# Optimization experiments

Measured on AMD Instinct MI355X. Metric: run time of the kernel, lower is better.

The kernel has to match this reference:

```python
import jax, jax.numpy as jnp
import numpy as np

Q = 4096   # query_size = argument_size*relation_size*position_size = 32*16*8
L = 8192   # number of context rows


def setup_inputs() -> dict:
    key = jax.random.key(0)
    k1, k2, k3 = jax.random.split(key, 3)
    query = jax.random.normal(k1, (Q,), dtype=jnp.float32)
    context_vector = jax.random.normal(k2, (L, Q), dtype=jnp.float32)
    # torch Linear(2Q, Q, bias=False): weight shape [Q, 2Q], scaled init
    K_w = jax.random.normal(k3, (Q, 2 * Q), dtype=jnp.float32) / np.sqrt(2 * Q)
    return {"query": query, "context_vector": context_vector, "K_w": K_w}


def reference(query, context_vector, K_w):
    # score[l] = <context_vector[l], query>  -> [L]
    score = context_vector @ query
    attention = jax.nn.softmax(score, axis=0)          # softmax over L
    s_t = attention @ context_vector                    # [Q]
    gamma = jnp.concatenate([query, s_t])               # [2Q]
    return K_w @ gamma                                   # Linear(2Q -> Q), no bias
```

## Files before the change

### kernel.cpp

```cpp
#include <hip/hip_runtime.h>

#define Q 4096
#define L 8192

__global__ __launch_bounds__(256) void score_kernel(
    const float* __restrict__ ctx, const float* __restrict__ qvec,
    float* __restrict__ score)
{
    const int lane = threadIdx.x & 63;
    const int w    = blockIdx.x * 4 + (threadIdx.x >> 6);
    const float4* __restrict__ row = (const float4*)(ctx + (size_t)w * Q);
    const float4* __restrict__ qv  = (const float4*)qvec;

    float a0 = 0.f, a1 = 0.f, a2 = 0.f, a3 = 0.f;
    #pragma unroll
    for (int c = 0; c < 16; c += 4) {
        float4 x0 = row[(c + 0) * 64 + lane], y0 = qv[(c + 0) * 64 + lane];
        float4 x1 = row[(c + 1) * 64 + lane], y1 = qv[(c + 1) * 64 + lane];
        float4 x2 = row[(c + 2) * 64 + lane], y2 = qv[(c + 2) * 64 + lane];
        float4 x3 = row[(c + 3) * 64 + lane], y3 = qv[(c + 3) * 64 + lane];
        a0 = fmaf(x0.x, y0.x, a0); a0 = fmaf(x0.y, y0.y, a0);
        a0 = fmaf(x0.z, y0.z, a0); a0 = fmaf(x0.w, y0.w, a0);
        a1 = fmaf(x1.x, y1.x, a1); a1 = fmaf(x1.y, y1.y, a1);
        a1 = fmaf(x1.z, y1.z, a1); a1 = fmaf(x1.w, y1.w, a1);
        a2 = fmaf(x2.x, y2.x, a2); a2 = fmaf(x2.y, y2.y, a2);
        a2 = fmaf(x2.z, y2.z, a2); a2 = fmaf(x2.w, y2.w, a2);
        a3 = fmaf(x3.x, y3.x, a3); a3 = fmaf(x3.y, y3.y, a3);
        a3 = fmaf(x3.z, y3.z, a3); a3 = fmaf(x3.w, y3.w, a3);
    }
    float d = (a0 + a1) + (a2 + a3);
    #pragma unroll
    for (int off = 32; off > 0; off >>= 1) d += __shfl_down(d, off, 64);
    if (lane == 0) score[w] = d;
}

__global__ __launch_bounds__(1024) void softmax_kernel(
    const float* __restrict__ score, float* __restrict__ att)
{
    __shared__ float redm[16];
    __shared__ float reds[16];
    const int tid  = threadIdx.x;
    const int lane = tid & 63;
    const int wid  = tid >> 6;

    float m = -3.4e38f;
    for (int i = tid; i < L; i += 1024) m = fmaxf(m, score[i]);
    #pragma unroll
    for (int off = 32; off > 0; off >>= 1) m = fmaxf(m, __shfl_down(m, off, 64));
    if (lane == 0) redm[wid] = m;
    __syncthreads();
    float M = redm[0];
    #pragma unroll
    for (int w = 1; w < 16; ++w) M = fmaxf(M, redm[w]);

    float s = 0.f;
    for (int i = tid; i < L; i += 1024) s += __expf(score[i] - M);
    #pragma unroll
    for (int off = 32; off > 0; off >>= 1) s += __shfl_down(s, off, 64);
    if (lane == 0) reds[wid] = s;
    __syncthreads();
    float Z = 0.f;
    #pragma unroll
    for (int w = 0; w < 16; ++w) Z += reds[w];
    const float inv = 1.0f / Z;

    for (int i = tid; i < L; i += 1024) att[i] = __expf(score[i] - M) * inv;
}

__global__ __launch_bounds__(256) void wsum_kernel(
    const float* __restrict__ ctx, const float* __restrict__ att,
    float* __restrict__ partial)
{
    __shared__ float att_s[64];
    const int cc  = blockIdx.x & 3;
    const int rc  = blockIdx.x >> 2;
    const int tid = threadIdx.x;
    const int col = cc * 256 + tid;

    if (tid < 64) att_s[tid] = att[rc * 64 + tid];
    __syncthreads();

    const float4* __restrict__ cb = (const float4*)ctx;
    const int r0 = rc * 64;
    float4 acc = make_float4(0.f, 0.f, 0.f, 0.f);
    #pragma unroll 8
    for (int r = 0; r < 64; ++r) {
        const float a = att_s[r];
        float4 v = cb[(size_t)(r0 + r) * (Q / 4) + col];
        acc.x = fmaf(a, v.x, acc.x);
        acc.y = fmaf(a, v.y, acc.y);
        acc.z = fmaf(a, v.z, acc.z);
        acc.w = fmaf(a, v.w, acc.w);
    }
    ((float4*)partial)[(size_t)rc * (Q / 4) + col] = acc;
}

__global__ __launch_bounds__(256) void reduce_kernel(
    const float* __restrict__ partial, float* __restrict__ s_t)
{
    const int c4 = blockIdx.x * 256 + threadIdx.x;
    const float4* __restrict__ p = (const float4*)partial;
    float4 acc = make_float4(0.f, 0.f, 0.f, 0.f);
    #pragma unroll 8
    for (int b = 0; b < 128; ++b) {
        float4 v = p[(size_t)b * (Q / 4) + c4];
        acc.x += v.x; acc.y += v.y; acc.z += v.z; acc.w += v.w;
    }
    ((float4*)s_t)[c4] = acc;
}

__global__ __launch_bounds__(256) void out_kernel(
    const float* __restrict__ Kw, const float* __restrict__ qvec,
    const float* __restrict__ s_t, float* __restrict__ out)
{
    const int lane = threadIdx.x & 63;
    const int i    = blockIdx.x * 4 + (threadIdx.x >> 6);
    const float4* __restrict__ row = (const float4*)(Kw + (size_t)i * (2 * Q));
    const float4* __restrict__ qv  = (const float4*)qvec;
    const float4* __restrict__ sv  = (const float4*)s_t;

    float a0 = 0.f, a1 = 0.f, a2 = 0.f, a3 = 0.f;
    #pragma unroll
    for (int c = 0; c < 16; c += 4) {
        float4 x0 = row[(c + 0) * 64 + lane], y0 = qv[(c + 0) * 64 + lane];
        float4 x1 = row[(c + 1) * 64 + lane], y1 = qv[(c + 1) * 64 + lane];
        float4 x2 = row[(c + 2) * 64 + lane], y2 = qv[(c + 2) * 64 + lane];
        float4 x3 = row[(c + 3) * 64 + lane], y3 = qv[(c + 3) * 64 + lane];
        a0 = fmaf(x0.x, y0.x, a0); a0 = fmaf(x0.y, y0.y, a0);
        a0 = fmaf(x0.z, y0.z, a0); a0 = fmaf(x0.w, y0.w, a0);
        a1 = fmaf(x1.x, y1.x, a1); a1 = fmaf(x1.y, y1.y, a1);
        a1 = fmaf(x1.z, y1.z, a1); a1 = fmaf(x1.w, y1.w, a1);
        a2 = fmaf(x2.x, y2.x, a2); a2 = fmaf(x2.y, y2.y, a2);
        a2 = fmaf(x2.z, y2.z, a2); a2 = fmaf(x2.w, y2.w, a2);
        a3 = fmaf(x3.x, y3.x, a3); a3 = fmaf(x3.y, y3.y, a3);
        a3 = fmaf(x3.z, y3.z, a3); a3 = fmaf(x3.w, y3.w, a3);
    }
    #pragma unroll
    for (int c = 0; c < 16; c += 4) {
        float4 x0 = row[(16 + c + 0) * 64 + lane], y0 = sv[(c + 0) * 64 + lane];
        float4 x1 = row[(16 + c + 1) * 64 + lane], y1 = sv[(c + 1) * 64 + lane];
        float4 x2 = row[(16 + c + 2) * 64 + lane], y2 = sv[(c + 2) * 64 + lane];
        float4 x3 = row[(16 + c + 3) * 64 + lane], y3 = sv[(c + 3) * 64 + lane];
        a0 = fmaf(x0.x, y0.x, a0); a0 = fmaf(x0.y, y0.y, a0);
        a0 = fmaf(x0.z, y0.z, a0); a0 = fmaf(x0.w, y0.w, a0);
        a1 = fmaf(x1.x, y1.x, a1); a1 = fmaf(x1.y, y1.y, a1);
        a1 = fmaf(x1.z, y1.z, a1); a1 = fmaf(x1.w, y1.w, a1);
        a2 = fmaf(x2.x, y2.x, a2); a2 = fmaf(x2.y, y2.y, a2);
        a2 = fmaf(x2.z, y2.z, a2); a2 = fmaf(x2.w, y2.w, a2);
        a3 = fmaf(x3.x, y3.x, a3); a3 = fmaf(x3.y, y3.y, a3);
        a3 = fmaf(x3.z, y3.z, a3); a3 = fmaf(x3.w, y3.w, a3);
    }
    float d = (a0 + a1) + (a2 + a3);
    #pragma unroll
    for (int off = 32; off > 0; off >>= 1) d += __shfl_down(d, off, 64);
    if (lane == 0) out[i] = d;
}

extern "C" void kernel_launch(void* const* d_in, const int* in_sizes, int n_in,
                              void* d_out, int out_size, void* d_ws, size_t ws_size,
                              hipStream_t stream)
{
    const float* query = (const float*)d_in[0];
    const float* ctx   = (const float*)d_in[1];
    const float* Kw    = (const float*)d_in[2];
    float* out = (float*)d_out;

    float* ws      = (float*)d_ws;
    float* score   = ws;
    float* att     = ws + L;
    float* s_t     = ws + 2 * L;
    float* partial = ws + 2 * L + Q;

    score_kernel<<<2048, 256, 0, stream>>>(ctx, query, score);
    softmax_kernel<<<1, 1024, 0, stream>>>(score, att);
    wsum_kernel<<<512, 256, 0, stream>>>(ctx, att, partial);
    reduce_kernel<<<4, 256, 0, stream>>>(partial, s_t);
    out_kernel<<<1024, 256, 0, stream>>>(Kw, query, s_t, out);
}
```

Measured before the change: 83.16 us.

## Fuse softmax into chunked weighted-sum with online max and merge kernel

Removes the single-block softmax kernel by having each weighted-sum block compute a local max and exp-weights over 16 rows, storing per-block max and sum. A new merge kernel rescales and reduces the partials and normalizes. Rows are processed in four chunks, interleaving score and wsum so the second context read can hit cache. This adds more launches and a larger partial buffer to reduce.

```diff
diff --git a/kernel.cpp b/kernel.cpp
--- a/kernel.cpp
+++ b/kernel.cpp
@@ -2,13 +2,18 @@
 
 #define Q 4096
 #define L 8192
+#define NCHUNK 4
+#define CROWS (L / NCHUNK)
+#define WROWS 16
+#define NPB (L / WROWS)
+#define WCB 4
 
 __global__ __launch_bounds__(256) void score_kernel(
     const float* __restrict__ ctx, const float* __restrict__ qvec,
-    float* __restrict__ score)
+    float* __restrict__ score, int r0base)
 {
     const int lane = threadIdx.x & 63;
-    const int w    = blockIdx.x * 4 + (threadIdx.x >> 6);
+    const int w    = r0base + blockIdx.x * 4 + (threadIdx.x >> 6);
     const float4* __restrict__ row = (const float4*)(ctx + (size_t)w * Q);
     const float4* __restrict__ qv  = (const float4*)qvec;
 
@@ -34,79 +39,102 @@
     if (lane == 0) score[w] = d;
 }
 
-__global__ __launch_bounds__(1024) void softmax_kernel(
-    const float* __restrict__ score, float* __restrict__ att)
-{
-    __shared__ float redm[16];
-    __shared__ float reds[16];
-    const int tid  = threadIdx.x;
-    const int lane = tid & 63;
-    const int wid  = tid >> 6;
-
-    float m = -3.4e38f;
-    for (int i = tid; i < L; i += 1024) m = fmaxf(m, score[i]);
-    #pragma unroll
-    for (int off = 32; off > 0; off >>= 1) m = fmaxf(m, __shfl_down(m, off, 64));
-    if (lane == 0) redm[wid] = m;
-    __syncthreads();
-    float M = redm[0];
-    #pragma unroll
-    for (int w = 1; w < 16; ++w) M = fmaxf(M, redm[w]);
-
-    float s = 0.f;
-    for (int i = tid; i < L; i += 1024) s += __expf(score[i] - M);
-    #pragma unroll
-    for (int off = 32; off > 0; off >>= 1) s += __shfl_down(s, off, 64);
-    if (lane == 0) reds[wid] = s;
-    __syncthreads();
-    float Z = 0.f;
-    #pragma unroll
-    for (int w = 0; w < 16; ++w) Z += reds[w];
-    const float inv = 1.0f / Z;
-
-    for (int i = tid; i < L; i += 1024) att[i] = __expf(score[i] - M) * inv;
-}
-
 __global__ __launch_bounds__(256) void wsum_kernel(
-    const float* __restrict__ ctx, const float* __restrict__ att,
-    float* __restrict__ partial)
-{
-    __shared__ float att_s[64];
-    const int cc  = blockIdx.x & 3;
-    const int rc  = blockIdx.x >> 2;
+    const float* __restrict__ ctx, const float* __restrict__ score,
+    float* __restrict__ partial, float* __restrict__ m_arr,
+    float* __restrict__ Z_arr, int r0base)
+{
+    __shared__ float sc_s[WROWS];
+    __shared__ float w_s[WROWS];
+    const int cc  = blockIdx.x & (WCB - 1);
+    const int rg  = blockIdx.x / WCB;
+    const int r0  = r0base + rg * WROWS;
+    const int pb  = r0 / WROWS;
     const int tid = threadIdx.x;
+
+    if (tid < WROWS) sc_s[tid] = score[r0 + tid];
+    __syncthreads();
+    float m = sc_s[0];
+    #pragma unroll
+    for (int r = 1; r < WROWS; ++r) m = fmaxf(m, sc_s[r]);
+    if (tid < WROWS) w_s[tid] = __expf(sc_s[tid] - m);
+    __syncthreads();
+
     const int col = cc * 256 + tid;
-
-    if (tid < 64) att_s[tid] = att[rc * 64 + tid];
-    __syncthreads();
-
     const float4* __restrict__ cb = (const float4*)ctx;
-    const int r0 = rc * 64;
     float4 acc = make_float4(0.f, 0.f, 0.f, 0.f);
-    #pragma unroll 8
-    for (int r = 0; r < 64; ++r) {
-        const float a = att_s[r];
+    #pragma unroll
+    for (int r = 0; r < WROWS; ++r) {
+        const float a = w_s[r];
         float4 v = cb[(size_t)(r0 + r) * (Q / 4) + col];
         acc.x = fmaf(a, v.x, acc.x);
         acc.y = fmaf(a, v.y, acc.y);
         acc.z = fmaf(a, v.z, acc.z);
         acc.w = fmaf(a, v.w, acc.w);
     }
-    ((float4*)partial)[(size_t)rc * (Q / 4) + col] = acc;
-}
-
-__global__ __launch_bounds__(256) void reduce_kernel(
-    const float* __restrict__ partial, float* __restrict__ s_t)
-{
-    const int c4 = blockIdx.x * 256 + threadIdx.x;
+    ((float4*)partial)[(size_t)pb * (Q / 4) + col] = acc;
+
+    if (cc == 0 && tid == 0) {
+        float Z = 0.f;
+        #pragma unroll
+        for (int r = 0; r < WROWS; ++r) Z += w_s[r];
+        m_arr[pb] = m;
+        Z_arr[pb] = Z;
+    }
+}
+
+__global__ __launch_bounds__(256) void merge_kernel(
+    const float* __restrict__ partial, const float* __restrict__ m_arr,
+    const float* __restrict__ Z_arr, float* __restrict__ s_t)
+{
+    __shared__ float wc[NPB];
+    __shared__ float red[4];
+    __shared__ float4 sacc[16][16];
+    const int tid  = threadIdx.x;
+    const int lane = tid & 63;
+    const int wid  = tid >> 6;
+
+    float mv = fmaxf(m_arr[tid], m_arr[tid + 256]);
+    #pragma unroll
+    for (int off = 32; off > 0; off >>= 1) mv = fmaxf(mv, __shfl_down(mv, off, 64));
+    if (lane == 0) red[wid] = mv;
+    __syncthreads();
+    const float M = fmaxf(fmaxf(red[0], red[1]), fmaxf(red[2], red[3]));
+    __syncthreads();
+
+    const float w0 = __expf(m_arr[tid] - M);
+    const float w1 = __expf(m_arr[tid + 256] - M);
+    wc[tid] = w0; wc[tid + 256] = w1;
+    float zv = fmaf(w0, Z_arr[tid], w1 * Z_arr[tid + 256]);
+    #pragma unroll
+    for (int off = 32; off > 0; off >>= 1) zv += __shfl_down(zv, off, 64);
+    if (lane == 0) red[wid] = zv;
+    __syncthreads();
+    const float invZ = 1.f / (red[0] + red[1] + red[2] + red[3]);
+
+    const int cidx = tid & 15;
+    const int g    = tid >> 4;
+    const int c4   = blockIdx.x * 16 + cidx;
     const float4* __restrict__ p = (const float4*)partial;
     float4 acc = make_float4(0.f, 0.f, 0.f, 0.f);
-    #pragma unroll 8
-    for (int b = 0; b < 128; ++b) {
+    for (int b = g; b < NPB; b += 16) {
+        const float w = wc[b];
         float4 v = p[(size_t)b * (Q / 4) + c4];
-        acc.x += v.x; acc.y += v.y; acc.z += v.z; acc.w += v.w;
-    }
-    ((float4*)s_t)[c4] = acc;
+        acc.x = fmaf(w, v.x, acc.x); acc.y = fmaf(w, v.y, acc.y);
+        acc.z = fmaf(w, v.z, acc.z); acc.w = fmaf(w, v.w, acc.w);
+    }
+    sacc[g][cidx] = acc;
+    __syncthreads();
+    if (g == 0) {
+        float4 t = sacc[0][cidx];
+        #pragma unroll
+        for (int gg = 1; gg < 16; ++gg) {
+            float4 u = sacc[gg][cidx];
+            t.x += u.x; t.y += u.y; t.z += u.z; t.w += u.w;
+        }
+        t.x *= invZ; t.y *= invZ; t.z *= invZ; t.w *= invZ;
+        ((float4*)s_t)[c4] = t;
+    }
 }
 
 __global__ __launch_bounds__(256) void out_kernel(
@@ -167,13 +195,17 @@
 
     float* ws      = (float*)d_ws;
     float* score   = ws;
-    float* att     = ws + L;
-    float* s_t     = ws + 2 * L;
-    float* partial = ws + 2 * L + Q;
-
-    score_kernel<<<2048, 256, 0, stream>>>(ctx, query, score);
-    softmax_kernel<<<1, 1024, 0, stream>>>(score, att);
-    wsum_kernel<<<512, 256, 0, stream>>>(ctx, att, partial);
-    reduce_kernel<<<4, 256, 0, stream>>>(partial, s_t);
-    out_kernel<<<1024, 256, 0, stream>>>(Kw, query, s_t, out);
-}
+    float* m_arr   = ws + L;
+    float* Z_arr   = ws + L + NPB;
+    float* s_t     = ws + L + 2 * NPB;
+    float* partial = ws + L + 2 * NPB + Q;
+
+    for (int c = 0; c < NCHUNK; ++c) {
+        const int r0 = c * CROWS;
+        score_kernel<<<CROWS / 4, 256, 0, stream>>>(ctx, query, score, r0);
+        wsum_kernel<<<(CROWS / WROWS) * WCB, 256, 0, stream>>>(
+            ctx, score, partial, m_arr, Z_arr, r0);
+    }
+    merge_kernel<<<Q / 4 / 16, 256, 0, stream>>>(partial, m_arr, Z_arr, s_t);
+    out_kernel<<<Q / 4, 256, 0, stream>>>(Kw, query, s_t, out);
+}
```

After: 86.34 us. +3.8%, slower.

## Stage query vectors in LDS, halve wsum row chunk, parallelize partial reduction

Applied to the files above, without the earlier changes.

The score and output GEMV kernels now stage the shared query (and s_t) vectors in LDS once per block instead of each wave re-reading them from global memory. The weighted-sum kernel processes 32 rows per block instead of 64, doubling the block count for more parallelism but producing twice as many partial rows. The reduce kernel now uses 16 blocks, with four wave groups per block splitting the 256 partials and combining them through LDS, instead of 4 blocks of serial 128-row loops. This adds LDS traffic and barriers, and doubles the partial buffer writes and reads.

```diff
diff --git a/kernel.cpp b/kernel.cpp
--- a/kernel.cpp
+++ b/kernel.cpp
@@ -7,18 +7,26 @@
     const float* __restrict__ ctx, const float* __restrict__ qvec,
     float* __restrict__ score)
 {
-    const int lane = threadIdx.x & 63;
-    const int w    = blockIdx.x * 4 + (threadIdx.x >> 6);
+    __shared__ float4 qs[Q / 4];
+    const int tid  = threadIdx.x;
+    const int lane = tid & 63;
+    const int wid  = tid >> 6;
+    const float4* __restrict__ qv = (const float4*)qvec;
+
+    #pragma unroll
+    for (int k = 0; k < 4; ++k) qs[tid + k * 256] = qv[tid + k * 256];
+    __syncthreads();
+
+    const int w = blockIdx.x * 4 + wid;
     const float4* __restrict__ row = (const float4*)(ctx + (size_t)w * Q);
-    const float4* __restrict__ qv  = (const float4*)qvec;
 
     float a0 = 0.f, a1 = 0.f, a2 = 0.f, a3 = 0.f;
     #pragma unroll
     for (int c = 0; c < 16; c += 4) {
-        float4 x0 = row[(c + 0) * 64 + lane], y0 = qv[(c + 0) * 64 + lane];
-        float4 x1 = row[(c + 1) * 64 + lane], y1 = qv[(c + 1) * 64 + lane];
-        float4 x2 = row[(c + 2) * 64 + lane], y2 = qv[(c + 2) * 64 + lane];
-        float4 x3 = row[(c + 3) * 64 + lane], y3 = qv[(c + 3) * 64 + lane];
+        float4 x0 = row[(c + 0) * 64 + lane], y0 = qs[(c + 0) * 64 + lane];
+        float4 x1 = row[(c + 1) * 64 + lane], y1 = qs[(c + 1) * 64 + lane];
+        float4 x2 = row[(c + 2) * 64 + lane], y2 = qs[(c + 2) * 64 + lane];
+        float4 x3 = row[(c + 3) * 64 + lane], y3 = qs[(c + 3) * 64 + lane];
         a0 = fmaf(x0.x, y0.x, a0); a0 = fmaf(x0.y, y0.y, a0);
         a0 = fmaf(x0.z, y0.z, a0); a0 = fmaf(x0.w, y0.w, a0);
         a1 = fmaf(x1.x, y1.x, a1); a1 = fmaf(x1.y, y1.y, a1);
@@ -71,20 +79,20 @@
     const float* __restrict__ ctx, const float* __restrict__ att,
     float* __restrict__ partial)
 {
-    __shared__ float att_s[64];
+    __shared__ float att_s[32];
     const int cc  = blockIdx.x & 3;
     const int rc  = blockIdx.x >> 2;
     const int tid = threadIdx.x;
     const int col = cc * 256 + tid;
 
-    if (tid < 64) att_s[tid] = att[rc * 64 + tid];
+    if (tid < 32) att_s[tid] = att[rc * 32 + tid];
     __syncthreads();
 
     const float4* __restrict__ cb = (const float4*)ctx;
-    const int r0 = rc * 64;
+    const int r0 = rc * 32;
     float4 acc = make_float4(0.f, 0.f, 0.f, 0.f);
     #pragma unroll 8
-    for (int r = 0; r < 64; ++r) {
+    for (int r = 0; r < 32; ++r) {
         const float a = att_s[r];
         float4 v = cb[(size_t)(r0 + r) * (Q / 4) + col];
         acc.x = fmaf(a, v.x, acc.x);
@@ -98,49 +106,56 @@
 __global__ __launch_bounds__(256) void reduce_kernel(
     const float* __restrict__ partial, float* __restrict__ s_t)
 {
-    const int c4 = blockIdx.x * 256 + threadIdx.x;
+    __shared__ float4 sacc[4][64];
+    const int c  = threadIdx.x & 63;
+    const int g  = threadIdx.x >> 6;
+    const int c4 = blockIdx.x * 64 + c;
     const float4* __restrict__ p = (const float4*)partial;
+
     float4 acc = make_float4(0.f, 0.f, 0.f, 0.f);
-    #pragma unroll 8
-    for (int b = 0; b < 128; ++b) {
+    for (int b = g; b < 256; b += 4) {
         float4 v = p[(size_t)b * (Q / 4) + c4];
         acc.x += v.x; acc.y += v.y; acc.z += v.z; acc.w += v.w;
     }
-    ((float4*)s_t)[c4] = acc;
+    sacc[g][c] = acc;
+    __syncthreads();
+    if (g == 0) {
+        float4 t = sacc[0][c], u1 = sacc[1][c], u2 = sacc[2][c], u3 = sacc[3][c];
+        t.x += u1.x + u2.x + u3.x;
+        t.y += u1.y + u2.y + u3.y;
+        t.z += u1.z + u2.z + u3.z;
+        t.w += u1.w + u2.w + u3.w;
+        ((float4*)s_t)[c4] = t;
+    }
 }
 
 __global__ __launch_bounds__(256) void out_kernel(
     const float* __restrict__ Kw, const float* __restrict__ qvec,
     const float* __restrict__ s_t, float* __restrict__ out)
 {
-    const int lane = threadIdx.x & 63;
-    const int i    = blockIdx.x * 4 + (threadIdx.x >> 6);
+    __shared__ float4 gs[2 * Q / 4];
+    const int tid  = threadIdx.x;
+    const int lane = tid & 63;
+    const int wid  = tid >> 6;
+    const float4* __restrict__ qv = (const float4*)qvec;
+    const float4* __restrict__ sv = (const float4*)s_t;
+
+    #pragma unroll
+    for (int k = 0; k < 4; ++k) gs[tid + k * 256] = qv[tid + k * 256];
+    #pragma unroll
+    for (int k = 0; k < 4; ++k) gs[1024 + tid + k * 256] = sv[tid + k * 256];
+    __syncthreads();
+
+    const int i = blockIdx.x * 4 + wid;
     const float4* __restrict__ row = (const float4*)(Kw + (size_t)i * (2 * Q));
-    const float4* __restrict__ qv  = (const float4*)qvec;
-    const float4* __restrict__ sv  = (const float4*)s_t;
 
     float a0 = 0.f, a1 = 0.f, a2 = 0.f, a3 = 0.f;
     #pragma unroll
-    for (int c = 0; c < 16; c += 4) {
-        float4 x0 = row[(c + 0) * 64 + lane], y0 = qv[(c + 0) * 64 + lane];
-        float4 x1 = row[(c + 1) * 64 + lane], y1 = qv[(c + 1) * 64 + lane];
-        float4 x2 = row[(c + 2) * 64 + lane], y2 = qv[(c + 2) * 64 + lane];
-        float4 x3 = row[(c + 3) * 64 + lane], y3 = qv[(c + 3) * 64 + lane];
-        a0 = fmaf(x0.x, y0.x, a0); a0 = fmaf(x0.y, y0.y, a0);
-        a0 = fmaf(x0.z, y0.z, a0); a0 = fmaf(x0.w, y0.w, a0);
-        a1 = fmaf(x1.x, y1.x, a1); a1 = fmaf(x1.y, y1.y, a1);
-        a1 = fmaf(x1.z, y1.z, a1); a1 = fmaf(x1.w, y1.w, a1);
-        a2 = fmaf(x2.x, y2.x, a2); a2 = fmaf(x2.y, y2.y, a2);
-        a2 = fmaf(x2.z, y2.z, a2); a2 = fmaf(x2.w, y2.w, a2);
-        a3 = fmaf(x3.x, y3.x, a3); a3 = fmaf(x3.y, y3.y, a3);
-        a3 = fmaf(x3.z, y3.z, a3); a3 = fmaf(x3.w, y3.w, a3);
-    }
-    #pragma unroll
-    for (int c = 0; c < 16; c += 4) {
-        float4 x0 = row[(16 + c + 0) * 64 + lane], y0 = sv[(c + 0) * 64 + lane];
-        float4 x1 = row[(16 + c + 1) * 64 + lane], y1 = sv[(c + 1) * 64 + lane];
-        float4 x2 = row[(16 + c + 2) * 64 + lane], y2 = sv[(c + 2) * 64 + lane];
-        float4 x3 = row[(16 + c + 3) * 64 + lane], y3 = sv[(c + 3) * 64 + lane];
+    for (int c = 0; c < 32; c += 4) {
+        float4 x0 = row[(c + 0) * 64 + lane], y0 = gs[(c + 0) * 64 + lane];
+        float4 x1 = row[(c + 1) * 64 + lane], y1 = gs[(c + 1) * 64 + lane];
+        float4 x2 = row[(c + 2) * 64 + lane], y2 = gs[(c + 2) * 64 + lane];
+        float4 x3 = row[(c + 3) * 64 + lane], y3 = gs[(c + 3) * 64 + lane];
         a0 = fmaf(x0.x, y0.x, a0); a0 = fmaf(x0.y, y0.y, a0);
         a0 = fmaf(x0.z, y0.z, a0); a0 = fmaf(x0.w, y0.w, a0);
         a1 = fmaf(x1.x, y1.x, a1); a1 = fmaf(x1.y, y1.y, a1);
@@ -171,9 +186,9 @@
     float* s_t     = ws + 2 * L;
     float* partial = ws + 2 * L + Q;
 
-    score_kernel<<<2048, 256, 0, stream>>>(ctx, query, score);
+    score_kernel<<<L / 4, 256, 0, stream>>>(ctx, query, score);
     softmax_kernel<<<1, 1024, 0, stream>>>(score, att);
-    wsum_kernel<<<512, 256, 0, stream>>>(ctx, att, partial);
-    reduce_kernel<<<4, 256, 0, stream>>>(partial, s_t);
-    out_kernel<<<1024, 256, 0, stream>>>(Kw, query, s_t, out);
+    wsum_kernel<<<1024, 256, 0, stream>>>(ctx, att, partial);
+    reduce_kernel<<<Q / 4 / 64, 256, 0, stream>>>(partial, s_t);
+    out_kernel<<<Q / 4, 256, 0, stream>>>(Kw, query, s_t, out);
 }
```

New measurement: 90.90 us. +9.3%, slower.
